# Kernel optimization log

Measured on AMD Instinct MI355X. Metric: run time of the kernel, lower is better.

The kernel has to match this reference:

```python
import jax, jax.numpy as jnp
import numpy as np

IN, H = 512, 1024
EPS = 1e-5

def _ln(x, g, b):
    mu = jnp.mean(x, axis=-1, keepdims=True)
    var = jnp.mean(jnp.square(x - mu), axis=-1, keepdims=True)
    return (x - mu) * jax.lax.rsqrt(var + EPS) * g + b

def setup_inputs() -> dict:
    key = jax.random.key(0)
    ks = jax.random.split(key, 8)
    B = 8192
    x = jax.random.normal(ks[0], (B, IN), jnp.float32)
    h_prev = jax.random.normal(ks[1], (B, H), jnp.float32)
    c_prev = jax.random.normal(ks[2], (B, H), jnp.float32)
    # Xavier-uniform weights (torch Linear: weight [out, in])
    lim_i = float(np.sqrt(6.0 / (IN + 4 * H)))
    lim_h = float(np.sqrt(6.0 / (H + 4 * H)))
    Wi = jax.random.uniform(ks[3], (4 * H, IN), jnp.float32, -lim_i, lim_i)
    Wh = jax.random.uniform(ks[4], (4 * H, H), jnp.float32, -lim_h, lim_h)
    # biases zero-ish with forget-gate slice set to 1.0 (matches _initialize_weights)
    bi = jnp.zeros((4 * H,), jnp.float32).at[H:2 * H].set(1.0)
    bh = jnp.zeros((4 * H,), jnp.float32).at[H:2 * H].set(1.0)
    g_in = jnp.ones((4 * H,), jnp.float32); b_in = jnp.zeros((4 * H,), jnp.float32)
    g_hid = jnp.ones((4 * H,), jnp.float32); b_hid = jnp.zeros((4 * H,), jnp.float32)
    g_cell = jnp.ones((H,), jnp.float32); b_cell = jnp.zeros((H,), jnp.float32)
    return {"x": x, "h_prev": h_prev, "c_prev": c_prev,
            "Wi": Wi, "bi": bi, "Wh": Wh, "bh": bh,
            "g_in": g_in, "b_in": b_in, "g_hid": g_hid, "b_hid": b_hid,
            "g_cell": g_cell, "b_cell": b_cell}

def reference(x, h_prev, c_prev, Wi, bi, Wh, bh, g_in, b_in, g_hid, b_hid, g_cell, b_cell):
    input_proj = _ln(x @ Wi.T + bi, g_in, b_in)          # [B, 4H]
    hidden_proj = _ln(h_prev @ Wh.T + bh, g_hid, b_hid)  # [B, 4H]
    combined = input_proj + hidden_proj
    i, f, g, o = jnp.split(combined, 4, axis=1)
    i = jax.nn.sigmoid(i); f = jax.nn.sigmoid(f)
    g = jnp.tanh(g); o = jax.nn.sigmoid(o)
    c_new = f * c_prev + i * g
    h_new = o * jnp.tanh(_ln(c_new, g_cell, b_cell))
    return (h_new, c_new)
```

## Files before the change

kernel.cpp:

```cpp
#include <hip/hip_runtime.h>
#include <hip/hip_bf16.h>

#define EPS 1e-5f

typedef __attribute__((ext_vector_type(8))) short short8;
typedef __attribute__((ext_vector_type(4))) float floatx4;

__device__ inline float b2f(short s) {
    union { unsigned u; float f; } v;
    v.u = ((unsigned)(unsigned short)s) << 16;
    return v.f;
}
__device__ inline float sigmoidf_(float x) { return 1.f / (1.f + __expf(-x)); }
__device__ inline float tanhf_(float x) { return 1.f - 2.f / (__expf(2.f * x) + 1.f); }

__device__ inline void load_lds16(const void* g, void* l) {
    __builtin_amdgcn_global_load_lds(
        (const __attribute__((address_space(1))) void*)g,
        (__attribute__((address_space(3))) void*)l, 16, 0, 0);
}

__global__ __launch_bounds__(256)
void cvt_bf16(const float* __restrict__ s0, __hip_bfloat16* __restrict__ d0,
              const float* __restrict__ s1, __hip_bfloat16* __restrict__ d1,
              const float* __restrict__ s2, __hip_bfloat16* __restrict__ d2,
              const float* __restrict__ s3, __hip_bfloat16* __restrict__ d3) {
    const int b = blockIdx.x;
    const float* s; __hip_bfloat16* d; int off;
    if (b < 2048)      { s = s0; d = d0; off = b; }
    else if (b < 6144) { s = s1; d = d1; off = b - 2048; }
    else if (b < 7168) { s = s2; d = d2; off = b - 6144; }
    else               { s = s3; d = d3; off = b - 7168; }
    const int idx = (off * 256 + threadIdx.x) * 8;
    float4 v0 = *(const float4*)(s + idx);
    float4 v1 = *(const float4*)(s + idx + 4);
    union { short8 sv; __hip_bfloat16 h[8]; } u;
    u.h[0] = __float2bfloat16(v0.x); u.h[1] = __float2bfloat16(v0.y);
    u.h[2] = __float2bfloat16(v0.z); u.h[3] = __float2bfloat16(v0.w);
    u.h[4] = __float2bfloat16(v1.x); u.h[5] = __float2bfloat16(v1.y);
    u.h[6] = __float2bfloat16(v1.z); u.h[7] = __float2bfloat16(v1.w);
    *(short8*)(d + idx) = u.sv;
}

__global__ __launch_bounds__(256, 3)
void gemm_dual(const __hip_bfloat16* __restrict__ A0, const __hip_bfloat16* __restrict__ W0,
               const float* __restrict__ bias0, __hip_bfloat16* __restrict__ out0, int K0,
               const __hip_bfloat16* __restrict__ A1, const __hip_bfloat16* __restrict__ W1,
               const float* __restrict__ bias1, __hip_bfloat16* __restrict__ out1, int K1) {
    __shared__ alignas(16) __hip_bfloat16 smem[17408];
    __hip_bfloat16* sA = smem;
    __hip_bfloat16* sB = smem + 8192;

    const __hip_bfloat16* A;  const __hip_bfloat16* W;
    const float* bias;        __hip_bfloat16* out;  int K;
    if (blockIdx.z == 0) { A = A0; W = W0; bias = bias0; out = out0; K = K0; }
    else                 { A = A1; W = W1; bias = bias1; out = out1; K = K1; }

    const int t    = threadIdx.x;
    const int lane = t & 63;
    const int wave = t >> 6;
    const int quad = lane >> 4;
    const int rl   = lane & 15;
    const int wm   = (wave >> 1) * 64;
    const int wn   = (wave & 1) * 64;
    const int m0   = blockIdx.y * 128;
    const int n0   = blockIdx.x * 128;

    floatx4 acc[4][4];
    #pragma unroll
    for (int i = 0; i < 4; ++i)
        #pragma unroll
        for (int j = 0; j < 4; ++j)
            acc[i][j] = (floatx4){0.f, 0.f, 0.f, 0.f};

    int srow[4], scol[4];
    #pragma unroll
    for (int i = 0; i < 4; ++i) {
        const int cl  = (wave * 4 + i) * 64 + lane;
        const int row = cl >> 3;
        srow[i] = row;
        scol[i] = ((cl & 7) ^ (row & 7)) * 8;
    }

    for (int k0 = 0; k0 < K; k0 += 64) {
        __syncthreads();
        #pragma unroll
        for (int i = 0; i < 4; ++i) {
            load_lds16(A + (size_t)(m0 + srow[i]) * K + k0 + scol[i], sA + (wave * 4 + i) * 512);
            load_lds16(W + (size_t)(n0 + srow[i]) * K + k0 + scol[i], sB + (wave * 4 + i) * 512);
        }
        __syncthreads();
        #pragma unroll
        for (int kk = 0; kk < 2; ++kk) {
            short8 aF[4], bF[4];
            #pragma unroll
            for (int i = 0; i < 4; ++i) {
                const int r = wm + i * 16 + rl;
                const int c = kk * 4 + quad;
                aF[i] = *(const short8*)(sA + (r * 8 + (c ^ (r & 7))) * 8);
            }
            #pragma unroll
            for (int j = 0; j < 4; ++j) {
                const int r = wn + j * 16 + rl;
                const int c = kk * 4 + quad;
                bF[j] = *(const short8*)(sB + (r * 8 + (c ^ (r & 7))) * 8);
            }
            #pragma unroll
            for (int i = 0; i < 4; ++i)
                #pragma unroll
                for (int j = 0; j < 4; ++j)
                    acc[i][j] = __builtin_amdgcn_mfma_f32_16x16x32_bf16(aF[i], bF[j], acc[i][j], 0, 0, 0);
        }
    }

    __syncthreads();
    #pragma unroll
    for (int j = 0; j < 4; ++j) {
        const int col = wn + j * 16 + rl;
        const float bv = bias[n0 + col];
        #pragma unroll
        for (int i = 0; i < 4; ++i) {
            const int rbase = wm + i * 16 + quad * 4;
            #pragma unroll
            for (int r = 0; r < 4; ++r)
                smem[(rbase + r) * 136 + col] = __float2bfloat16(acc[i][j][r] + bv);
        }
    }
    __syncthreads();
    #pragma unroll
    for (int p = 0; p < 8; ++p) {
        const int ch  = p * 256 + t;
        const int row = ch >> 4;
        const int c8  = (ch & 15) * 8;
        short8 v = *(const short8*)(smem + row * 136 + c8);
        *(short8*)(out + (size_t)(m0 + row) * 4096 + n0 + c8) = v;
    }
}

__global__ __launch_bounds__(512)
void ln_gates(const __hip_bfloat16* __restrict__ Pi, const __hip_bfloat16* __restrict__ Ph,
              const float* __restrict__ c_prev,
              const float* __restrict__ g_in, const float* __restrict__ b_in,
              const float* __restrict__ g_hid, const float* __restrict__ b_hid,
              const float* __restrict__ g_cell, const float* __restrict__ b_cell,
              float* __restrict__ h_out, float* __restrict__ c_out) {
    const int t    = threadIdx.x;
    const int rid  = t >> 7;
    const int tt   = t & 127;
    const int wave = t >> 6;
    const int row  = blockIdx.x * 4 + rid;
    __shared__ float sred[8][6];

    const __hip_bfloat16* pi = Pi + (size_t)row * 4096;
    const __hip_bfloat16* ph = Ph + (size_t)row * 4096;
    const int j0 = tt * 8;

    float fpi[4][8], fph[4][8];
    float si = 0.f, sqi = 0.f, sh = 0.f, sqh = 0.f;
    #pragma unroll
    for (int g = 0; g < 4; ++g) {
        short8 vi = *(const short8*)(pi + g * 1024 + j0);
        short8 vh = *(const short8*)(ph + g * 1024 + j0);
        #pragma unroll
        for (int e = 0; e < 8; ++e) {
            const float a = b2f(vi[e]); fpi[g][e] = a; si += a; sqi += a * a;
            const float b = b2f(vh[e]); fph[g][e] = b; sh += b; sqh += b * b;
        }
    }
    floatx4 cp0 = *(const floatx4*)(c_prev + (size_t)row * 1024 + j0);
    floatx4 cp1 = *(const floatx4*)(c_prev + (size_t)row * 1024 + j0 + 4);

    #pragma unroll
    for (int mask = 1; mask <= 32; mask <<= 1) {
        si += __shfl_xor(si, mask); sqi += __shfl_xor(sqi, mask);
        sh += __shfl_xor(sh, mask); sqh += __shfl_xor(sqh, mask);
    }
    if ((t & 63) == 0) {
        sred[wave][0] = si; sred[wave][1] = sqi;
        sred[wave][2] = sh; sred[wave][3] = sqh;
    }
    __syncthreads();
    const int wb = rid * 2;
    si  = sred[wb][0] + sred[wb + 1][0];
    sqi = sred[wb][1] + sred[wb + 1][1];
    sh  = sred[wb][2] + sred[wb + 1][2];
    sqh = sred[wb][3] + sred[wb + 1][3];

    const float mu_i = si * (1.f / 4096.f);
    const float rs_i = rsqrtf(sqi * (1.f / 4096.f) - mu_i * mu_i + EPS);
    const float mu_h = sh * (1.f / 4096.f);
    const float rs_h = rsqrtf(sqh * (1.f / 4096.f) - mu_h * mu_h + EPS);

    float comb[4][8];
    #pragma unroll
    for (int g = 0; g < 4; ++g) {
        const int col = g * 1024 + j0;
        floatx4 gi0  = *(const floatx4*)(g_in  + col);
        floatx4 gi1  = *(const floatx4*)(g_in  + col + 4);
        floatx4 bi0  = *(const floatx4*)(b_in  + col);
        floatx4 bi1  = *(const floatx4*)(b_in  + col + 4);
        floatx4 gh0  = *(const floatx4*)(g_hid + col);
        floatx4 gh1  = *(const floatx4*)(g_hid + col + 4);
        floatx4 bh0  = *(const floatx4*)(b_hid + col);
        floatx4 bh1  = *(const floatx4*)(b_hid + col + 4);
        #pragma unroll
        for (int e = 0; e < 4; ++e) {
            comb[g][e]     = (fpi[g][e]     - mu_i) * rs_i * gi0[e] + bi0[e]
                           + (fph[g][e]     - mu_h) * rs_h * gh0[e] + bh0[e];
            comb[g][e + 4] = (fpi[g][e + 4] - mu_i) * rs_i * gi1[e] + bi1[e]
                           + (fph[g][e + 4] - mu_h) * rs_h * gh1[e] + bh1[e];
        }
    }

    float cn[8], ov[8];
    float sc = 0.f, scq = 0.f;
    #pragma unroll
    for (int e = 0; e < 8; ++e) {
        const float iv = sigmoidf_(comb[0][e]);
        const float fv = sigmoidf_(comb[1][e]);
        const float gv = tanhf_(comb[2][e]);
        ov[e] = sigmoidf_(comb[3][e]);
        const float cpv = (e < 4) ? cp0[e] : cp1[e - 4];
        const float c = fv * cpv + iv * gv;
        cn[e] = c; sc += c; scq += c * c;
    }
    #pragma unroll
    for (int mask = 1; mask <= 32; mask <<= 1) {
        sc += __shfl_xor(sc, mask); scq += __shfl_xor(scq, mask);
    }
    if ((t & 63) == 0) { sred[wave][4] = sc; sred[wave][5] = scq; }
    __syncthreads();
    sc  = sred[wb][4] + sred[wb + 1][4];
    scq = sred[wb][5] + sred[wb + 1][5];
    const float mu_c = sc * (1.f / 1024.f);
    const float rs_c = rsqrtf(scq * (1.f / 1024.f) - mu_c * mu_c + EPS);

    floatx4 gc0 = *(const floatx4*)(g_cell + j0);
    floatx4 gc1 = *(const floatx4*)(g_cell + j0 + 4);
    floatx4 bc0 = *(const floatx4*)(b_cell + j0);
    floatx4 bc1 = *(const floatx4*)(b_cell + j0 + 4);
    floatx4 hv0, hv1, cv0, cv1;
    #pragma unroll
    for (int e = 0; e < 4; ++e) {
        const float nc0 = (cn[e]     - mu_c) * rs_c * gc0[e] + bc0[e];
        const float nc1 = (cn[e + 4] - mu_c) * rs_c * gc1[e] + bc1[e];
        hv0[e] = ov[e] * tanhf_(nc0);
        hv1[e] = ov[e + 4] * tanhf_(nc1);
        cv0[e] = cn[e];
        cv1[e] = cn[e + 4];
    }
    float* hp = h_out + (size_t)row * 1024 + j0;
    float* cpout = c_out + (size_t)row * 1024 + j0;
    *(floatx4*)(hp) = hv0;     *(floatx4*)(hp + 4) = hv1;
    *(floatx4*)(cpout) = cv0;  *(floatx4*)(cpout + 4) = cv1;
}

extern "C" void kernel_launch(void* const* d_in, const int* in_sizes, int n_in,
                              void* d_out, int out_size, void* d_ws, size_t ws_size,
                              hipStream_t stream) {
    const float* x      = (const float*)d_in[0];
    const float* h_prev = (const float*)d_in[1];
    const float* c_prev = (const float*)d_in[2];
    const float* Wi     = (const float*)d_in[3];
    const float* bi     = (const float*)d_in[4];
    const float* Wh     = (const float*)d_in[5];
    const float* bh     = (const float*)d_in[6];
    const float* g_in   = (const float*)d_in[7];
    const float* b_in   = (const float*)d_in[8];
    const float* g_hid  = (const float*)d_in[9];
    const float* b_hid  = (const float*)d_in[10];
    const float* g_cell = (const float*)d_in[11];
    const float* b_cell = (const float*)d_in[12];

    __hip_bfloat16* Pi = (__hip_bfloat16*)d_ws;
    __hip_bfloat16* Ph = Pi + (size_t)8192 * 4096;

    const int NX = 8192 * 512, NH = 8192 * 1024;
    __hip_bfloat16* xb  = (__hip_bfloat16*)d_out;
    __hip_bfloat16* hb  = xb + NX;
    __hip_bfloat16* Wib = hb + NH;
    __hip_bfloat16* Whb = Wib + 4096 * 512;

    float* h_out = (float*)d_out;
    float* c_out = h_out + (size_t)8192 * 1024;

    hipLaunchKernelGGL(cvt_bf16, dim3(9216), dim3(256), 0, stream,
                       x, xb, h_prev, hb, Wi, Wib, Wh, Whb);

    hipLaunchKernelGGL(gemm_dual, dim3(32, 64, 2), dim3(256), 0, stream,
                       xb, Wib, bi, Pi, 512,
                       hb, Whb, bh, Ph, 1024);

    hipLaunchKernelGGL(ln_gates, dim3(2048), dim3(512), 0, stream, Pi, Ph, c_prev,
                       g_in, b_in, g_hid, b_hid, g_cell, b_cell, h_out, c_out);
}
```

Baseline: 310.0 us.

## Fuse convert, GEMM and LN-gate stages into one persistent kernel with grid barriers

Replaces the three launches (bf16 conversion, dual GEMM, LayerNorm and gates) with one persistent kernel of 768 blocks that walks through each stage and uses atomic grid barriers between them. GEMM tiles are split statically, 4 tiles of the K=1024 hidden GEMM per block for 512 blocks and 8 tiles of the K=512 input GEMM per block for the rest, to balance work. The aim is to remove launch gaps and inter-kernel tails. It relies on all 768 blocks being resident at once, otherwise the spin barrier deadlocks. The LN stage now uses 256-thread blocks with 2 rows each and keeps bf16 values in registers instead of float arrays. A workspace size check falls back to the old three-kernel path.

```diff
diff --git a/kernel.cpp b/kernel.cpp
--- a/kernel.cpp
+++ b/kernel.cpp
@@ -2,6 +2,7 @@
 #include <hip/hip_bf16.h>
 
 #define EPS 1e-5f
+#define NBLK 768
 
 typedef __attribute__((ext_vector_type(8))) short short8;
 typedef __attribute__((ext_vector_type(4))) float floatx4;
@@ -18,6 +19,280 @@
     __builtin_amdgcn_global_load_lds(
         (const __attribute__((address_space(1))) void*)g,
         (__attribute__((address_space(3))) void*)l, 16, 0, 0);
+}
+
+__device__ __forceinline__ void gridbar(unsigned* c) {
+    __threadfence();
+    __syncthreads();
+    if (threadIdx.x == 0) {
+        atomicAdd(c, 1u);
+        while (atomicAdd(c, 0u) < NBLK) __builtin_amdgcn_s_sleep(2);
+    }
+    __syncthreads();
+    __threadfence();
+}
+
+__device__ __forceinline__ void gemm_tile(
+    const __hip_bfloat16* __restrict__ A, const __hip_bfloat16* __restrict__ W,
+    const float* __restrict__ bias, __hip_bfloat16* __restrict__ out,
+    int K, int m0, int n0, __hip_bfloat16* smem)
+{
+    __hip_bfloat16* sA = smem;
+    __hip_bfloat16* sB = smem + 8192;
+    const int t    = threadIdx.x;
+    const int lane = t & 63;
+    const int wave = t >> 6;
+    const int quad = lane >> 4;
+    const int rl   = lane & 15;
+    const int wm   = (wave >> 1) * 64;
+    const int wn   = (wave & 1) * 64;
+
+    floatx4 acc[4][4];
+    #pragma unroll
+    for (int i = 0; i < 4; ++i)
+        #pragma unroll
+        for (int j = 0; j < 4; ++j)
+            acc[i][j] = (floatx4){0.f, 0.f, 0.f, 0.f};
+
+    int srow[4], scol[4];
+    #pragma unroll
+    for (int i = 0; i < 4; ++i) {
+        const int cl  = (wave * 4 + i) * 64 + lane;
+        const int row = cl >> 3;
+        srow[i] = row;
+        scol[i] = ((cl & 7) ^ (row & 7)) * 8;
+    }
+
+    for (int k0 = 0; k0 < K; k0 += 64) {
+        __syncthreads();
+        #pragma unroll
+        for (int i = 0; i < 4; ++i) {
+            load_lds16(A + (size_t)(m0 + srow[i]) * K + k0 + scol[i], sA + (wave * 4 + i) * 512);
+            load_lds16(W + (size_t)(n0 + srow[i]) * K + k0 + scol[i], sB + (wave * 4 + i) * 512);
+        }
+        __syncthreads();
+        #pragma unroll
+        for (int kk = 0; kk < 2; ++kk) {
+            short8 aF[4], bF[4];
+            #pragma unroll
+            for (int i = 0; i < 4; ++i) {
+                const int r = wm + i * 16 + rl;
+                const int c = kk * 4 + quad;
+                aF[i] = *(const short8*)(sA + (r * 8 + (c ^ (r & 7))) * 8);
+            }
+            #pragma unroll
+            for (int j = 0; j < 4; ++j) {
+                const int r = wn + j * 16 + rl;
+                const int c = kk * 4 + quad;
+                bF[j] = *(const short8*)(sB + (r * 8 + (c ^ (r & 7))) * 8);
+            }
+            #pragma unroll
+            for (int i = 0; i < 4; ++i)
+                #pragma unroll
+                for (int j = 0; j < 4; ++j)
+                    acc[i][j] = __builtin_amdgcn_mfma_f32_16x16x32_bf16(aF[i], bF[j], acc[i][j], 0, 0, 0);
+        }
+    }
+
+    __syncthreads();
+    #pragma unroll
+    for (int j = 0; j < 4; ++j) {
+        const int col = wn + j * 16 + rl;
+        const float bv = bias[n0 + col];
+        #pragma unroll
+        for (int i = 0; i < 4; ++i) {
+            const int rbase = wm + i * 16 + quad * 4;
+            #pragma unroll
+            for (int r = 0; r < 4; ++r)
+                smem[(rbase + r) * 136 + col] = __float2bfloat16(acc[i][j][r] + bv);
+        }
+    }
+    __syncthreads();
+    #pragma unroll
+    for (int p = 0; p < 8; ++p) {
+        const int ch  = p * 256 + t;
+        const int row = ch >> 4;
+        const int c8  = (ch & 15) * 8;
+        short8 v = *(const short8*)(smem + row * 136 + c8);
+        *(short8*)(out + (size_t)(m0 + row) * 4096 + n0 + c8) = v;
+    }
+}
+
+__device__ __forceinline__ void ln2rows(
+    int vb, const __hip_bfloat16* __restrict__ Pi, const __hip_bfloat16* __restrict__ Ph,
+    const float* __restrict__ c_prev,
+    const float* __restrict__ g_in, const float* __restrict__ b_in,
+    const float* __restrict__ g_hid, const float* __restrict__ b_hid,
+    const float* __restrict__ g_cell, const float* __restrict__ b_cell,
+    float* __restrict__ h_out, float* __restrict__ c_out, float* sredf)
+{
+    const int t    = threadIdx.x;
+    const int half = t >> 7;
+    const int tt   = t & 127;
+    const int wave = t >> 6;
+    const int row  = vb * 2 + half;
+
+    const __hip_bfloat16* pi = Pi + (size_t)row * 4096;
+    const __hip_bfloat16* ph = Ph + (size_t)row * 4096;
+    const int j0 = tt * 8;
+
+    short8 vi[4], vh[4];
+    float si = 0.f, sqi = 0.f, sh = 0.f, sqh = 0.f;
+    #pragma unroll
+    for (int g = 0; g < 4; ++g) {
+        vi[g] = *(const short8*)(pi + g * 1024 + j0);
+        vh[g] = *(const short8*)(ph + g * 1024 + j0);
+        #pragma unroll
+        for (int e = 0; e < 8; ++e) {
+            const float a = b2f(vi[g][e]); si += a; sqi += a * a;
+            const float b = b2f(vh[g][e]); sh += b; sqh += b * b;
+        }
+    }
+    floatx4 cp0 = *(const floatx4*)(c_prev + (size_t)row * 1024 + j0);
+    floatx4 cp1 = *(const floatx4*)(c_prev + (size_t)row * 1024 + j0 + 4);
+
+    #pragma unroll
+    for (int mask = 1; mask <= 32; mask <<= 1) {
+        si += __shfl_xor(si, mask); sqi += __shfl_xor(sqi, mask);
+        sh += __shfl_xor(sh, mask); sqh += __shfl_xor(sqh, mask);
+    }
+    if ((t & 63) == 0) {
+        sredf[wave * 6 + 0] = si; sredf[wave * 6 + 1] = sqi;
+        sredf[wave * 6 + 2] = sh; sredf[wave * 6 + 3] = sqh;
+    }
+    __syncthreads();
+    const int wb = half * 2;
+    si  = sredf[wb * 6 + 0] + sredf[wb * 6 + 6];
+    sqi = sredf[wb * 6 + 1] + sredf[wb * 6 + 7];
+    sh  = sredf[wb * 6 + 2] + sredf[wb * 6 + 8];
+    sqh = sredf[wb * 6 + 3] + sredf[wb * 6 + 9];
+
+    const float mu_i = si * (1.f / 4096.f);
+    const float rs_i = rsqrtf(sqi * (1.f / 4096.f) - mu_i * mu_i + EPS);
+    const float mu_h = sh * (1.f / 4096.f);
+    const float rs_h = rsqrtf(sqh * (1.f / 4096.f) - mu_h * mu_h + EPS);
+
+    float comb[4][8];
+    #pragma unroll
+    for (int g = 0; g < 4; ++g) {
+        const int col = g * 1024 + j0;
+        floatx4 gi0  = *(const floatx4*)(g_in  + col);
+        floatx4 gi1  = *(const floatx4*)(g_in  + col + 4);
+        floatx4 bi0  = *(const floatx4*)(b_in  + col);
+        floatx4 bi1  = *(const floatx4*)(b_in  + col + 4);
+        floatx4 gh0  = *(const floatx4*)(g_hid + col);
+        floatx4 gh1  = *(const floatx4*)(g_hid + col + 4);
+        floatx4 bh0  = *(const floatx4*)(b_hid + col);
+        floatx4 bh1  = *(const floatx4*)(b_hid + col + 4);
+        #pragma unroll
+        for (int e = 0; e < 4; ++e) {
+            comb[g][e]     = (b2f(vi[g][e])     - mu_i) * rs_i * gi0[e] + bi0[e]
+                           + (b2f(vh[g][e])     - mu_h) * rs_h * gh0[e] + bh0[e];
+            comb[g][e + 4] = (b2f(vi[g][e + 4]) - mu_i) * rs_i * gi1[e] + bi1[e]
+                           + (b2f(vh[g][e + 4]) - mu_h) * rs_h * gh1[e] + bh1[e];
+        }
+    }
+
+    float cn[8], ov[8];
+    float sc = 0.f, scq = 0.f;
+    #pragma unroll
+    for (int e = 0; e < 8; ++e) {
+        const float iv = sigmoidf_(comb[0][e]);
+        const float fv = sigmoidf_(comb[1][e]);
+        const float gv = tanhf_(comb[2][e]);
+        ov[e] = sigmoidf_(comb[3][e]);
+        const float cpv = (e < 4) ? cp0[e] : cp1[e - 4];
+        const float c = fv * cpv + iv * gv;
+        cn[e] = c; sc += c; scq += c * c;
+    }
+    #pragma unroll
+    for (int mask = 1; mask <= 32; mask <<= 1) {
+        sc += __shfl_xor(sc, mask); scq += __shfl_xor(scq, mask);
+    }
+    if ((t & 63) == 0) { sredf[wave * 6 + 4] = sc; sredf[wave * 6 + 5] = scq; }
+    __syncthreads();
+    sc  = sredf[wb * 6 + 4] + sredf[wb * 6 + 10];
+    scq = sredf[wb * 6 + 5] + sredf[wb * 6 + 11];
+    const float mu_c = sc * (1.f / 1024.f);
+    const float rs_c = rsqrtf(scq * (1.f / 1024.f) - mu_c * mu_c + EPS);
+
+    floatx4 gc0 = *(const floatx4*)(g_cell + j0);
+    floatx4 gc1 = *(const floatx4*)(g_cell + j0 + 4);
+    floatx4 bc0 = *(const floatx4*)(b_cell + j0);
+    floatx4 bc1 = *(const floatx4*)(b_cell + j0 + 4);
+    floatx4 hv0, hv1, cv0, cv1;
+    #pragma unroll
+    for (int e = 0; e < 4; ++e) {
+        const float nc0 = (cn[e]     - mu_c) * rs_c * gc0[e] + bc0[e];
+        const float nc1 = (cn[e + 4] - mu_c) * rs_c * gc1[e] + bc1[e];
+        hv0[e] = ov[e] * tanhf_(nc0);
+        hv1[e] = ov[e + 4] * tanhf_(nc1);
+        cv0[e] = cn[e];
+        cv1[e] = cn[e + 4];
+    }
+    float* hp = h_out + (size_t)row * 1024 + j0;
+    float* cpout = c_out + (size_t)row * 1024 + j0;
+    *(floatx4*)(hp) = hv0;     *(floatx4*)(hp + 4) = hv1;
+    *(floatx4*)(cpout) = cv0;  *(floatx4*)(cpout + 4) = cv1;
+}
+
+__global__ __launch_bounds__(256, 3)
+void fused_cell(const float* __restrict__ x, const float* __restrict__ h_prev,
+                const float* __restrict__ c_prev,
+                const float* __restrict__ Wi, const float* __restrict__ bi,
+                const float* __restrict__ Wh, const float* __restrict__ bh,
+                const float* __restrict__ g_in, const float* __restrict__ b_in,
+                const float* __restrict__ g_hid, const float* __restrict__ b_hid,
+                const float* __restrict__ g_cell, const float* __restrict__ b_cell,
+                __hip_bfloat16* __restrict__ xb, __hip_bfloat16* __restrict__ hb,
+                __hip_bfloat16* __restrict__ Wib, __hip_bfloat16* __restrict__ Whb,
+                __hip_bfloat16* __restrict__ Pi, __hip_bfloat16* __restrict__ Ph,
+                float* __restrict__ h_out, float* __restrict__ c_out,
+                unsigned* __restrict__ bar)
+{
+    __shared__ alignas(16) __hip_bfloat16 smem[17408];
+    const int bid = blockIdx.x;
+
+    for (int it = 0; it < 12; ++it) {
+        const int v = bid + NBLK * it;
+        const float* s; __hip_bfloat16* d; int off;
+        if (v < 2048)      { s = x;      d = xb;  off = v; }
+        else if (v < 6144) { s = h_prev; d = hb;  off = v - 2048; }
+        else if (v < 7168) { s = Wi;     d = Wib; off = v - 6144; }
+        else               { s = Wh;     d = Whb; off = v - 7168; }
+        const int idx = (off * 256 + threadIdx.x) * 8;
+        float4 v0 = *(const float4*)(s + idx);
+        float4 v1 = *(const float4*)(s + idx + 4);
+        union { short8 sv; __hip_bfloat16 h[8]; } u;
+        u.h[0] = __float2bfloat16(v0.x); u.h[1] = __float2bfloat16(v0.y);
+        u.h[2] = __float2bfloat16(v0.z); u.h[3] = __float2bfloat16(v0.w);
+        u.h[4] = __float2bfloat16(v1.x); u.h[5] = __float2bfloat16(v1.y);
+        u.h[6] = __float2bfloat16(v1.z); u.h[7] = __float2bfloat16(v1.w);
+        *(short8*)(d + idx) = u.sv;
+    }
+    gridbar(bar);
+
+    if (bid < 512) {
+        #pragma unroll 1
+        for (int j = 0; j < 4; ++j) {
+            const int tile = bid * 4 + j;
+            gemm_tile(hb, Whb, bh, Ph, 1024, (tile >> 5) * 128, (tile & 31) * 128, smem);
+        }
+    } else {
+        #pragma unroll 1
+        for (int j = 0; j < 8; ++j) {
+            const int tile = (bid - 512) * 8 + j;
+            gemm_tile(xb, Wib, bi, Pi, 512, (tile >> 5) * 128, (tile & 31) * 128, smem);
+        }
+    }
+    gridbar(bar + 1);
+
+    for (int k = 0; k < 6; ++k) {
+        const int v = bid + NBLK * k;
+        if (v < 4096)
+            ln2rows(v, Pi, Ph, c_prev, g_in, b_in, g_hid, b_hid, g_cell, b_cell,
+                    h_out, c_out, (float*)smem);
+    }
 }
 
 __global__ __launch_bounds__(256)
@@ -48,211 +323,23 @@
                const __hip_bfloat16* __restrict__ A1, const __hip_bfloat16* __restrict__ W1,
                const float* __restrict__ bias1, __hip_bfloat16* __restrict__ out1, int K1) {
     __shared__ alignas(16) __hip_bfloat16 smem[17408];
-    __hip_bfloat16* sA = smem;
-    __hip_bfloat16* sB = smem + 8192;
-
     const __hip_bfloat16* A;  const __hip_bfloat16* W;
     const float* bias;        __hip_bfloat16* out;  int K;
     if (blockIdx.z == 0) { A = A0; W = W0; bias = bias0; out = out0; K = K0; }
     else                 { A = A1; W = W1; bias = bias1; out = out1; K = K1; }
-
-    const int t    = threadIdx.x;
-    const int lane = t & 63;
-    const int wave = t >> 6;
-    const int quad = lane >> 4;
-    const int rl   = lane & 15;
-    const int wm   = (wave >> 1) * 64;
-    const int wn   = (wave & 1) * 64;
-    const int m0   = blockIdx.y * 128;
-    const int n0   = blockIdx.x * 128;
-
-    floatx4 acc[4][4];
-    #pragma unroll
-    for (int i = 0; i < 4; ++i)
-        #pragma unroll
-        for (int j = 0; j < 4; ++j)
-            acc[i][j] = (floatx4){0.f, 0.f, 0.f, 0.f};
-
-    int srow[4], scol[4];
-    #pragma unroll
-    for (int i = 0; i < 4; ++i) {
-        const int cl  = (wave * 4 + i) * 64 + lane;
-        const int row = cl >> 3;
-        srow[i] = row;
-        scol[i] = ((cl & 7) ^ (row & 7)) * 8;
-    }
-
-    for (int k0 = 0; k0 < K; k0 += 64) {
-        __syncthreads();
-        #pragma unroll
-        for (int i = 0; i < 4; ++i) {
-            load_lds16(A + (size_t)(m0 + srow[i]) * K + k0 + scol[i], sA + (wave * 4 + i) * 512);
-            load_lds16(W + (size_t)(n0 + srow[i]) * K + k0 + scol[i], sB + (wave * 4 + i) * 512);
-        }
-        __syncthreads();
-        #pragma unroll
-        for (int kk = 0; kk < 2; ++kk) {
-            short8 aF[4], bF[4];
-            #pragma unroll
-            for (int i = 0; i < 4; ++i) {
-                const int r = wm + i * 16 + rl;
-                const int c = kk * 4 + quad;
-                aF[i] = *(const short8*)(sA + (r * 8 + (c ^ (r & 7))) * 8);
-            }
-            #pragma unroll
-            for (int j = 0; j < 4; ++j) {
-                const int r = wn + j * 16 + rl;
-                const int c = kk * 4 + quad;
-                bF[j] = *(const short8*)(sB + (r * 8 + (c ^ (r & 7))) * 8);
-            }
-            #pragma unroll
-            for (int i = 0; i < 4; ++i)
-                #pragma unroll
-                for (int j = 0; j < 4; ++j)
-                    acc[i][j] = __builtin_amdgcn_mfma_f32_16x16x32_bf16(aF[i], bF[j], acc[i][j], 0, 0, 0);
-        }
-    }
-
-    __syncthreads();
-    #pragma unroll
-    for (int j = 0; j < 4; ++j) {
-        const int col = wn + j * 16 + rl;
-        const float bv = bias[n0 + col];
-        #pragma unroll
-        for (int i = 0; i < 4; ++i) {
-            const int rbase = wm + i * 16 + quad * 4;
-            #pragma unroll
-            for (int r = 0; r < 4; ++r)
-                smem[(rbase + r) * 136 + col] = __float2bfloat16(acc[i][j][r] + bv);
-        }
-    }
-    __syncthreads();
-    #pragma unroll
-    for (int p = 0; p < 8; ++p) {
-        const int ch  = p * 256 + t;
-        const int row = ch >> 4;
-        const int c8  = (ch & 15) * 8;
-        short8 v = *(const short8*)(smem + row * 136 + c8);
-        *(short8*)(out + (size_t)(m0 + row) * 4096 + n0 + c8) = v;
-    }
-}
-
-__global__ __launch_bounds__(512)
+    gemm_tile(A, W, bias, out, K, blockIdx.y * 128, blockIdx.x * 128, smem);
+}
+
+__global__ __launch_bounds__(256)
 void ln_gates(const __hip_bfloat16* __restrict__ Pi, const __hip_bfloat16* __restrict__ Ph,
               const float* __restrict__ c_prev,
               const float* __restrict__ g_in, const float* __restrict__ b_in,
               const float* __restrict__ g_hid, const float* __restrict__ b_hid,
               const float* __restrict__ g_cell, const float* __restrict__ b_cell,
               float* __restrict__ h_out, float* __restrict__ c_out) {
-    const int t    = threadIdx.x;
-    const int rid  = t >> 7;
-    const int tt   = t & 127;
-    const int wave = t >> 6;
-    const int row  = blockIdx.x * 4 + rid;
-    __shared__ float sred[8][6];
-
-    const __hip_bfloat16* pi = Pi + (size_t)row * 4096;
-    const __hip_bfloat16* ph = Ph + (size_t)row * 4096;
-    const int j0 = tt * 8;
-
-    float fpi[4][8], fph[4][8];
-    float si = 0.f, sqi = 0.f, sh = 0.f, sqh = 0.f;
-    #pragma unroll
-    for (int g = 0; g < 4; ++g) {
-        short8 vi = *(const short8*)(pi + g * 1024 + j0);
-        short8 vh = *(const short8*)(ph + g * 1024 + j0);
-        #pragma unroll
-        for (int e = 0; e < 8; ++e) {
-            const float a = b2f(vi[e]); fpi[g][e] = a; si += a; sqi += a * a;
-            const float b = b2f(vh[e]); fph[g][e] = b; sh += b; sqh += b * b;
-        }
-    }
-    floatx4 cp0 = *(const floatx4*)(c_prev + (size_t)row * 1024 + j0);
-    floatx4 cp1 = *(const floatx4*)(c_prev + (size_t)row * 1024 + j0 + 4);
-
-    #pragma unroll
-    for (int mask = 1; mask <= 32; mask <<= 1) {
-        si += __shfl_xor(si, mask); sqi += __shfl_xor(sqi, mask);
-        sh += __shfl_xor(sh, mask); sqh += __shfl_xor(sqh, mask);
-    }
-    if ((t & 63) == 0) {
-        sred[wave][0] = si; sred[wave][1] = sqi;
-        sred[wave][2] = sh; sred[wave][3] = sqh;
-    }
-    __syncthreads();
-    const int wb = rid * 2;
-    si  = sred[wb][0] + sred[wb + 1][0];
-    sqi = sred[wb][1] + sred[wb + 1][1];
-    sh  = sred[wb][2] + sred[wb + 1][2];
-    sqh = sred[wb][3] + sred[wb + 1][3];
-
-    const float mu_i = si * (1.f / 4096.f);
-    const float rs_i = rsqrtf(sqi * (1.f / 4096.f) - mu_i * mu_i + EPS);
-    const float mu_h = sh * (1.f / 4096.f);
-    const float rs_h = rsqrtf(sqh * (1.f / 4096.f) - mu_h * mu_h + EPS);
-
-    float comb[4][8];
-    #pragma unroll
-    for (int g = 0; g < 4; ++g) {
-        const int col = g * 1024 + j0;
-        floatx4 gi0  = *(const floatx4*)(g_in  + col);
-        floatx4 gi1  = *(const floatx4*)(g_in  + col + 4);
-        floatx4 bi0  = *(const floatx4*)(b_in  + col);
-        floatx4 bi1  = *(const floatx4*)(b_in  + col + 4);
-        floatx4 gh0  = *(const floatx4*)(g_hid + col);
-        floatx4 gh1  = *(const floatx4*)(g_hid + col + 4);
-        floatx4 bh0  = *(const floatx4*)(b_hid + col);
-        floatx4 bh1  = *(const floatx4*)(b_hid + col + 4);
-        #pragma unroll
-        for (int e = 0; e < 4; ++e) {
-            comb[g][e]     = (fpi[g][e]     - mu_i) * rs_i * gi0[e] + bi0[e]
-                           + (fph[g][e]     - mu_h) * rs_h * gh0[e] + bh0[e];
-            comb[g][e + 4] = (fpi[g][e + 4] - mu_i) * rs_i * gi1[e] + bi1[e]
-                           + (fph[g][e + 4] - mu_h) * rs_h * gh1[e] + bh1[e];
-        }
-    }
-
-    float cn[8], ov[8];
-    float sc = 0.f, scq = 0.f;
-    #pragma unroll
-    for (int e = 0; e < 8; ++e) {
-        const float iv = sigmoidf_(comb[0][e]);
-        const float fv = sigmoidf_(comb[1][e]);
-        const float gv = tanhf_(comb[2][e]);
-        ov[e] = sigmoidf_(comb[3][e]);
-        const float cpv = (e < 4) ? cp0[e] : cp1[e - 4];
-        const float c = fv * cpv + iv * gv;
-        cn[e] = c; sc += c; scq += c * c;
-    }
-    #pragma unroll
-    for (int mask = 1; mask <= 32; mask <<= 1) {
-        sc += __shfl_xor(sc, mask); scq += __shfl_xor(scq, mask);
-    }
-    if ((t & 63) == 0) { sred[wave][4] = sc; sred[wave][5] = scq; }
-    __syncthreads();
-    sc  = sred[wb][4] + sred[wb + 1][4];
-    scq = sred[wb][5] + sred[wb + 1][5];
-    const float mu_c = sc * (1.f / 1024.f);
-    const float rs_c = rsqrtf(scq * (1.f / 1024.f) - mu_c * mu_c + EPS);
-
-    floatx4 gc0 = *(const floatx4*)(g_cell + j0);
-    floatx4 gc1 = *(const floatx4*)(g_cell + j0 + 4);
-    floatx4 bc0 = *(const floatx4*)(b_cell + j0);
-    floatx4 bc1 = *(const floatx4*)(b_cell + j0 + 4);
-    floatx4 hv0, hv1, cv0, cv1;
-    #pragma unroll
-    for (int e = 0; e < 4; ++e) {
-        const float nc0 = (cn[e]     - mu_c) * rs_c * gc0[e] + bc0[e];
-        const float nc1 = (cn[e + 4] - mu_c) * rs_c * gc1[e] + bc1[e];
-        hv0[e] = ov[e] * tanhf_(nc0);
-        hv1[e] = ov[e + 4] * tanhf_(nc1);
-        cv0[e] = cn[e];
-        cv1[e] = cn[e + 4];
-    }
-    float* hp = h_out + (size_t)row * 1024 + j0;
-    float* cpout = c_out + (size_t)row * 1024 + j0;
-    *(floatx4*)(hp) = hv0;     *(floatx4*)(hp + 4) = hv1;
-    *(floatx4*)(cpout) = cv0;  *(floatx4*)(cpout + 4) = cv1;
+    __shared__ float sredf[24];
+    ln2rows(blockIdx.x, Pi, Ph, c_prev, g_in, b_in, g_hid, b_hid, g_cell, b_cell,
+            h_out, c_out, sredf);
 }
 
 extern "C" void kernel_launch(void* const* d_in, const int* in_sizes, int n_in,
@@ -284,13 +371,21 @@
     float* h_out = (float*)d_out;
     float* c_out = h_out + (size_t)8192 * 1024;
 
-    hipLaunchKernelGGL(cvt_bf16, dim3(9216), dim3(256), 0, stream,
-                       x, xb, h_prev, hb, Wi, Wib, Wh, Whb);
-
-    hipLaunchKernelGGL(gemm_dual, dim3(32, 64, 2), dim3(256), 0, stream,
-                       xb, Wib, bi, Pi, 512,
-                       hb, Whb, bh, Ph, 1024);
-
-    hipLaunchKernelGGL(ln_gates, dim3(2048), dim3(512), 0, stream, Pi, Ph, c_prev,
-                       g_in, b_in, g_hid, b_hid, g_cell, b_cell, h_out, c_out);
-}
+    const size_t barOff = (size_t)134217728;
+    if (ws_size >= barOff + 16) {
+        unsigned* bar = (unsigned*)((char*)d_ws + barOff);
+        hipMemsetAsync(bar, 0, 16, stream);
+        hipLaunchKernelGGL(fused_cell, dim3(NBLK), dim3(256), 0, stream,
+                           x, h_prev, c_prev, Wi, bi, Wh, bh,
+                           g_in, b_in, g_hid, b_hid, g_cell, b_cell,
+                           xb, hb, Wib, Whb, Pi, Ph, h_out, c_out, bar);
+    } else {
+        hipLaunchKernelGGL(cvt_bf16, dim3(9216), dim3(256), 0, stream,
+                           x, xb, h_prev, hb, Wi, Wib, Wh, Whb);
+        hipLaunchKernelGGL(gemm_dual, dim3(32, 64, 2), dim3(256), 0, stream,
+                           xb, Wib, bi, Pi, 512,
+                           hb, Whb, bh, Ph, 1024);
+        hipLaunchKernelGGL(ln_gates, dim3(4096), dim3(256), 0, stream, Pi, Ph, c_prev,
+                           g_in, b_in, g_hid, b_hid, g_cell, b_cell, h_out, c_out);
+    }
+}
```

Result: slower. 701.6 us (+126.3%).
